# Performance work log

Measured on AMD Instinct MI355X. Metric: run time of the kernel, lower is better.

Reference implementation:

```python
import jax, jax.numpy as jnp
import numpy as np

BITS = 4
N_PACK = 8  # 32-bit container / 4-bit values
GROUPSIZE = 128
MASK = (1 << BITS) - 1


def _unpack(packed, n_valid):
    # packed: [R, ceil(n_valid/N_PACK)] int32 -> [R, n_valid] int32 nibbles
    shifts = (jnp.arange(N_PACK, dtype=jnp.int32) * BITS)
    vals = (packed[:, :, None] >> shifts) & MASK  # [R, C, N_PACK]
    return vals.reshape(packed.shape[0], -1)[:, :n_valid]


def setup_inputs() -> dict:
    key = jax.random.key(0)
    k0, k1, k2, k3, k4 = jax.random.split(key, 5)
    O, I = 4096, 4096
    ng = I // GROUPSIZE  # 32
    x = jax.random.normal(k0, (2, 2048, I), dtype=jnp.float32)
    packed_weight = jax.random.randint(k1, (O, I // N_PACK), 0, 2147483647, dtype=jnp.int32)
    scale = jax.random.uniform(k2, (O, ng), dtype=jnp.float32)
    packed_zp = jax.random.randint(k3, (O, (ng + N_PACK - 1) // N_PACK), 0, 2147483647, dtype=jnp.int32)
    bias = jax.random.normal(k4, (O,), dtype=jnp.float32)
    return {"x": x, "packed_weight": packed_weight, "scale": scale,
            "packed_zp": packed_zp, "bias": bias}


def reference(x, packed_weight, scale, packed_zp, bias):
    O, ng = scale.shape
    I = packed_weight.shape[1] * N_PACK
    # unpack uint4 weights and zero-points (matches torch recover(): shift+mask)
    w_int = _unpack(packed_weight, I)          # [O, I] values in [0, 15]
    zp_int = _unpack(packed_zp, ng)            # [O, ng]
    # per-group dequant: (w - zp) * scale
    w = w_int.reshape(O, ng, GROUPSIZE).astype(scale.dtype)
    fp_weight = ((w - zp_int[:, :, None].astype(scale.dtype)) * scale[:, :, None]).reshape(O, I)
    # F.linear: x @ W^T + b
    return jnp.einsum('bsi,oi->bso', x, fp_weight) + bias
```

## Files before the change

### kernel.cpp

```cpp
#include <hip/hip_runtime.h>
#include <stdint.h>

typedef __attribute__((ext_vector_type(4))) float  floatx4;
typedef __attribute__((ext_vector_type(8))) short  shortx8;
typedef __attribute__((ext_vector_type(4))) unsigned short ushortx4;

typedef unsigned int   u32;
typedef unsigned short u16;

#define TILE    128
#define BK      64
#define THREADS 256
#define CHUNK   (TILE * BK)

__device__ __forceinline__ u32 pack2bf(float f0, float f1) {
    u32 u0 = __builtin_bit_cast(u32, f0) + 0x8000u;
    u32 u1 = __builtin_bit_cast(u32, f1) + 0x8000u;
    return __builtin_amdgcn_perm(u1, u0, 0x07060302u);
}

__device__ __forceinline__ unsigned short f2bf(float f) {
    u32 u = __builtin_bit_cast(u32, f);
    u += 0x7FFFu + ((u >> 16) & 1u);
    return (unsigned short)(u >> 16);
}

__global__ __launch_bounds__(THREADS)
void prep_kernel(const float* __restrict__ x, const int* __restrict__ pw,
                 const float* __restrict__ scale, const int* __restrict__ pzp,
                 u16* __restrict__ At, u16* __restrict__ Bt,
                 int M, int O, int I, int ng, int lsSeg, int lsG) {
    const int NT = gridDim.x * THREADS;
    const int t0 = blockIdx.x * THREADS + threadIdx.x;
    const int segsPerRow = I >> 3;

    const int Sx = (M * I) >> 3;
    for (int s = t0; s < Sx; s += NT) {
        const float4 v0 = ((const float4*)x)[(size_t)s * 2];
        const float4 v1 = ((const float4*)x)[(size_t)s * 2 + 1];
        u32 p[4];
        p[0] = pack2bf(v0.x, v0.y); p[1] = pack2bf(v0.z, v0.w);
        p[2] = pack2bf(v1.x, v1.y); p[3] = pack2bf(v1.z, v1.w);
        ((uint4*)At)[s] = *(uint4*)p;
    }

    const int Sw = (O * I) >> 3;
    for (int s = t0; s < Sw; s += NT) {
        const u32 wq = (u32)pw[s];
        const int o    = s >> lsSeg;
        const int wcol = s & (segsPerRow - 1);
        const int g    = wcol >> lsG;
        const float sc = scale[o * ng + g];
        const int zpw  = pzp[o * ((ng + 7) >> 3) + (g >> 3)];
        const int zp   = (zpw >> ((g & 7) * 4)) & 15;
        const float nzc = -sc * (float)(zp + 128);
        float v[8];
        #pragma unroll
        for (int j = 0; j < 8; j++) {
            u32 tt;
            if (j < 4)       tt = (wq << (16 - 4 * j)) & 0x000F0000u;
            else if (j == 4) tt = wq & 0x000F0000u;
            else             tt = (wq >> (4 * j - 16)) & 0x000F0000u;
            v[j] = __builtin_fmaf(__builtin_bit_cast(float, tt | 0x43000000u), sc, nzc);
        }
        u32 p[4];
        p[0] = pack2bf(v[0], v[1]); p[1] = pack2bf(v[2], v[3]);
        p[2] = pack2bf(v[4], v[5]); p[3] = pack2bf(v[6], v[7]);
        ((uint4*)Bt)[s] = *(uint4*)p;
    }
}

__global__ __launch_bounds__(THREADS, 2)
void gemm_bf16(const u16* __restrict__ At, const u16* __restrict__ Bt,
               const float* __restrict__ bias, float* __restrict__ out,
               int O, int I, int KT) {
    __shared__ u16 As[CHUNK];
    __shared__ u16 Bs[CHUNK];

    const int tid = threadIdx.x;
    const int nblk_n = O / TILE;
    const int mt = blockIdx.x / nblk_n;
    const int nt = blockIdx.x % nblk_n;
    const int w = tid >> 6, lane = tid & 63;
    const int wm = w >> 1, wn = w & 1;
    const int l15 = lane & 15, l4 = lane >> 4;
    const int sw  = l15 & 7;

    const int sr = tid >> 3;
    const int sc = (tid & 7) ^ (sr & 7);

    floatx4 acc[4][4];
    #pragma unroll
    for (int i = 0; i < 4; i++)
        #pragma unroll
        for (int j = 0; j < 4; j++)
            acc[i][j] = (floatx4){0.f, 0.f, 0.f, 0.f};

    const u16* gaBase = At + ((size_t)(mt * TILE) + sr) * I + sc * 8;
    const u16* gbBase = Bt + ((size_t)(nt * TILE) + sr) * I + sc * 8;

    for (int kt = 0; kt < KT; kt++) {
        const u16* ga = gaBase + kt * BK;
        const u16* gb = gbBase + kt * BK;
        __syncthreads();
        #pragma unroll
        for (int it = 0; it < 4; it++) {
            const int ldsOff = it * 2048 + tid * 8;
            const size_t gOff = (size_t)(it * 32) * I;
            __builtin_amdgcn_global_load_lds((const __attribute__((address_space(1))) u32*)(ga + gOff),
                                             (__attribute__((address_space(3))) u32*)(As + ldsOff),
                                             16, 0, 0);
            __builtin_amdgcn_global_load_lds((const __attribute__((address_space(1))) u32*)(gb + gOff),
                                             (__attribute__((address_space(3))) u32*)(Bs + ldsOff),
                                             16, 0, 0);
        }
        __syncthreads();

        #pragma unroll
        for (int ks = 0; ks < 2; ks++) {
            shortx8 af[4], bf[4];
            #pragma unroll
            for (int i = 0; i < 4; i++)
                af[i] = *(const shortx8*)(&As[(wm * 64 + i * 16 + l15) * BK + ((ks * 4 + l4) ^ sw) * 8]);
            #pragma unroll
            for (int j = 0; j < 4; j++)
                bf[j] = *(const shortx8*)(&Bs[(wn * 64 + j * 16 + l15) * BK + ((ks * 4 + l4) ^ sw) * 8]);
            #pragma unroll
            for (int i = 0; i < 4; i++)
                #pragma unroll
                for (int j = 0; j < 4; j++)
                    acc[i][j] = __builtin_amdgcn_mfma_f32_16x16x32_bf16(af[i], bf[j], acc[i][j], 0, 0, 0);
        }
    }

    #pragma unroll
    for (int j = 0; j < 4; j++) {
        int col  = nt * TILE + wn * 64 + j * 16 + l15;
        float bv = bias[col];
        #pragma unroll
        for (int i = 0; i < 4; i++) {
            int rowb = mt * TILE + wm * 64 + i * 16 + l4 * 4;
            #pragma unroll
            for (int r = 0; r < 4; r++)
                out[(size_t)(rowb + r) * O + col] = acc[i][j][r] + bv;
        }
    }
}

#define LDA 72
__global__ __launch_bounds__(THREADS, 2)
void wql_fused(const float* __restrict__ x, const int* __restrict__ pw,
               const float* __restrict__ scale, const int* __restrict__ pzp,
               const float* __restrict__ bias, float* __restrict__ out,
               int M, int O, int I, int ng)
{
    __shared__ unsigned short As[TILE * LDA];
    __shared__ unsigned short Bs[TILE * LDA];
    const int tid = threadIdx.x;
    const int nblk_n = O / TILE;
    const int mt = blockIdx.x / nblk_n, nt = blockIdx.x % nblk_n;
    const int w = tid >> 6, lane = tid & 63;
    const int wm = w >> 1, wn = w & 1;
    const int l15 = lane & 15, l4 = lane >> 4;
    const int pw_rowlen = I / 8, zp_rowlen = (ng + 7) / 8, GS = I / ng;

    floatx4 acc[4][4];
    #pragma unroll
    for (int i = 0; i < 4; i++)
        #pragma unroll
        for (int j = 0; j < 4; j++) acc[i][j] = (floatx4){0.f, 0.f, 0.f, 0.f};

    const int nk = I / BK;
    for (int kt = 0; kt < nk; kt++) {
        __syncthreads();
        #pragma unroll
        for (int it = 0; it < 8; it++) {
            int f = tid + it * THREADS;
            int row = f >> 4, seg = f & 15;
            const float4 v = *(const float4*)(x + (size_t)(mt * TILE + row) * I + kt * BK + seg * 4);
            ushortx4 b;
            b.x = f2bf(v.x); b.y = f2bf(v.y); b.z = f2bf(v.z); b.w = f2bf(v.w);
            *(ushortx4*)(&As[row * LDA + seg * 4]) = b;
        }
        const int g = (kt * BK) / GS;
        #pragma unroll
        for (int it = 0; it < 4; it++) {
            int e = tid + it * THREADS;
            int row = e >> 3, c = e & 7;
            int o = nt * TILE + row;
            int wq = pw[(size_t)o * pw_rowlen + kt * (BK / 8) + c];
            float s = scale[o * ng + g];
            int zpw = pzp[o * zp_rowlen + (g >> 3)];
            int zp = (zpw >> ((g & 7) * 4)) & 15;
            shortx8 b;
            #pragma unroll
            for (int j = 0; j < 8; j++) {
                int nib = (wq >> (4 * j)) & 15;
                b[j] = (short)f2bf((float)(nib - zp) * s);
            }
            *(shortx8*)(&Bs[row * LDA + c * 8]) = b;
        }
        __syncthreads();
        #pragma unroll
        for (int ks = 0; ks < 2; ks++) {
            shortx8 af[4], bf[4];
            #pragma unroll
            for (int i = 0; i < 4; i++)
                af[i] = *(const shortx8*)(&As[(wm * 64 + i * 16 + l15) * LDA + ks * 32 + l4 * 8]);
            #pragma unroll
            for (int j = 0; j < 4; j++)
                bf[j] = *(const shortx8*)(&Bs[(wn * 64 + j * 16 + l15) * LDA + ks * 32 + l4 * 8]);
            #pragma unroll
            for (int i = 0; i < 4; i++)
                #pragma unroll
                for (int j = 0; j < 4; j++)
                    acc[i][j] = __builtin_amdgcn_mfma_f32_16x16x32_bf16(af[i], bf[j], acc[i][j], 0, 0, 0);
        }
    }
    #pragma unroll
    for (int j = 0; j < 4; j++) {
        int col = nt * TILE + wn * 64 + j * 16 + l15;
        float bv = bias[col];
        #pragma unroll
        for (int i = 0; i < 4; i++) {
            int rowb = mt * TILE + wm * 64 + i * 16 + l4 * 4;
            #pragma unroll
            for (int r = 0; r < 4; r++)
                out[(size_t)(rowb + r) * O + col] = acc[i][j][r] + bv;
        }
    }
}

extern "C" void kernel_launch(void* const* d_in, const int* in_sizes, int n_in,
                              void* d_out, int out_size, void* d_ws, size_t ws_size,
                              hipStream_t stream) {
    const float* x     = (const float*)d_in[0];
    const int*   pw    = (const int*)d_in[1];
    const float* scale = (const float*)d_in[2];
    const int*   pzp   = (const int*)d_in[3];
    const float* bias  = (const float*)d_in[4];
    float*       out   = (float*)d_out;

    const int O  = in_sizes[4];
    const int ng = in_sizes[2] / O;
    const int I  = (in_sizes[1] / O) * 8;
    const int M  = in_sizes[0] / I;
    const int KT = I / BK;
    int lsSeg = 0; { int v = I >> 3; while ((1 << lsSeg) < v) lsSeg++; }
    int lsG = 0;   { int v = (I / ng) >> 3; while ((1 << lsG) < v) lsG++; }

    const size_t need = ((size_t)M * I + (size_t)O * I) * sizeof(u16);
    if (ws_size >= need) {
        u16* At = (u16*)d_ws;
        u16* Bt = At + (size_t)M * I;
        prep_kernel<<<dim3(2048), THREADS, 0, stream>>>(x, pw, scale, pzp, At, Bt, M, O, I, ng, lsSeg, lsG);
        gemm_bf16<<<dim3((M / TILE) * (O / TILE)), THREADS, 0, stream>>>(At, Bt, bias, out, O, I, KT);
    } else {
        wql_fused<<<dim3((M / TILE) * (O / TILE)), THREADS, 0, stream>>>(x, pw, scale, pzp, bias, out, M, O, I, ng);
    }
}
```

Baseline: 252.8 us.

## Double-buffer LDS tiles in bf16 GEMM to overlap global loads with MFMA

The GEMM kernel gets two LDS buffers for A and B. It issues the direct-to-LDS loads for the next K tile before computing the current one, with a manual vmcnt wait and raw barriers. The aim is to hide global memory latency behind the MFMA work. LDS use doubles to 64KB per block, which may limit the two-blocks-per-CU occupancy, and the hand-written vmcnt count relies on exactly 8 outstanding loads per stage.

```diff
diff --git a/kernel.cpp b/kernel.cpp
--- a/kernel.cpp
+++ b/kernel.cpp
@@ -74,8 +74,8 @@
 void gemm_bf16(const u16* __restrict__ At, const u16* __restrict__ Bt,
                const float* __restrict__ bias, float* __restrict__ out,
                int O, int I, int KT) {
-    __shared__ u16 As[CHUNK];
-    __shared__ u16 Bs[CHUNK];
+    __shared__ u16 As[2][CHUNK];
+    __shared__ u16 Bs[2][CHUNK];
 
     const int tid = threadIdx.x;
     const int nblk_n = O / TILE;
@@ -98,40 +98,57 @@
 
     const u16* gaBase = At + ((size_t)(mt * TILE) + sr) * I + sc * 8;
     const u16* gbBase = Bt + ((size_t)(nt * TILE) + sr) * I + sc * 8;
-
-    for (int kt = 0; kt < KT; kt++) {
+    const int ldsOffBase = tid * 8;
+
+    auto issue = [&](int buf, int kt) {
         const u16* ga = gaBase + kt * BK;
         const u16* gb = gbBase + kt * BK;
-        __syncthreads();
         #pragma unroll
         for (int it = 0; it < 4; it++) {
-            const int ldsOff = it * 2048 + tid * 8;
+            const int ldsOff = it * 2048 + ldsOffBase;
             const size_t gOff = (size_t)(it * 32) * I;
             __builtin_amdgcn_global_load_lds((const __attribute__((address_space(1))) u32*)(ga + gOff),
-                                             (__attribute__((address_space(3))) u32*)(As + ldsOff),
+                                             (__attribute__((address_space(3))) u32*)(&As[buf][ldsOff]),
                                              16, 0, 0);
             __builtin_amdgcn_global_load_lds((const __attribute__((address_space(1))) u32*)(gb + gOff),
-                                             (__attribute__((address_space(3))) u32*)(Bs + ldsOff),
+                                             (__attribute__((address_space(3))) u32*)(&Bs[buf][ldsOff]),
                                              16, 0, 0);
         }
-        __syncthreads();
-
+    };
+
+    auto compute = [&](int buf) {
+        const u16* asb = As[buf];
+        const u16* bsb = Bs[buf];
         #pragma unroll
         for (int ks = 0; ks < 2; ks++) {
-            shortx8 af[4], bf[4];
-            #pragma unroll
-            for (int i = 0; i < 4; i++)
-                af[i] = *(const shortx8*)(&As[(wm * 64 + i * 16 + l15) * BK + ((ks * 4 + l4) ^ sw) * 8]);
+            shortx8 af[4], bfr[4];
+            #pragma unroll
+            for (int i = 0; i < 4; i++)
+                af[i] = *(const shortx8*)(&asb[(wm * 64 + i * 16 + l15) * BK + ((ks * 4 + l4) ^ sw) * 8]);
             #pragma unroll
             for (int j = 0; j < 4; j++)
-                bf[j] = *(const shortx8*)(&Bs[(wn * 64 + j * 16 + l15) * BK + ((ks * 4 + l4) ^ sw) * 8]);
+                bfr[j] = *(const shortx8*)(&bsb[(wn * 64 + j * 16 + l15) * BK + ((ks * 4 + l4) ^ sw) * 8]);
             #pragma unroll
             for (int i = 0; i < 4; i++)
                 #pragma unroll
                 for (int j = 0; j < 4; j++)
-                    acc[i][j] = __builtin_amdgcn_mfma_f32_16x16x32_bf16(af[i], bf[j], acc[i][j], 0, 0, 0);
-        }
-    }
+                    acc[i][j] = __builtin_amdgcn_mfma_f32_16x16x32_bf16(af[i], bfr[j], acc[i][j], 0, 0, 0);
+        }
+    };
+
+    issue(0, 0);
+    int cur = 0;
+    for (int kt = 0; kt < KT - 1; kt++) {
+        issue(cur ^ 1, kt + 1);
+        asm volatile("s_waitcnt vmcnt(8)" ::: "memory");
+        __builtin_amdgcn_s_barrier();
+        compute(cur);
+        __builtin_amdgcn_s_barrier();
+        cur ^= 1;
+    }
+    asm volatile("s_waitcnt vmcnt(0)" ::: "memory");
+    __builtin_amdgcn_s_barrier();
+    compute(cur);
 
     #pragma unroll
     for (int j = 0; j < 4; j++) {
@@ -203,18 +220,18 @@
         __syncthreads();
         #pragma unroll
         for (int ks = 0; ks < 2; ks++) {
-            shortx8 af[4], bf[4];
+            shortx8 af[4], bfr[4];
             #pragma unroll
             for (int i = 0; i < 4; i++)
                 af[i] = *(const shortx8*)(&As[(wm * 64 + i * 16 + l15) * LDA + ks * 32 + l4 * 8]);
             #pragma unroll
             for (int j = 0; j < 4; j++)
-                bf[j] = *(const shortx8*)(&Bs[(wn * 64 + j * 16 + l15) * LDA + ks * 32 + l4 * 8]);
+                bfr[j] = *(const shortx8*)(&Bs[(wn * 64 + j * 16 + l15) * LDA + ks * 32 + l4 * 8]);
             #pragma unroll
             for (int i = 0; i < 4; i++)
                 #pragma unroll
                 for (int j = 0; j < 4; j++)
-                    acc[i][j] = __builtin_amdgcn_mfma_f32_16x16x32_bf16(af[i], bf[j], acc[i][j], 0, 0, 0);
+                    acc[i][j] = __builtin_amdgcn_mfma_f32_16x16x32_bf16(af[i], bfr[j], acc[i][j], 0, 0, 0);
         }
     }
     #pragma unroll
```

New measurement: 269.2 us. +6.5%, slower.

## Add 256x256-tile 512-thread GEMM with 4-stage LDS pipeline and XCD block remap

Applied to the files above, without the earlier changes.

Adds a new bf16 GEMM kernel using 256x256 output tiles, 8 waves and a 4-deep LDS ring buffer. Async global-to-LDS loads for future k-steps are issued between MFMA phases, with explicit vmcnt waits, split barriers and s_setprio raised around the MFMA blocks. Block IDs are remapped so that groups of eight consecutive workgroups land on the same XCD's tile neighbourhood to improve L2 reuse. The larger tile lowers global traffic per FLOP and the deep pipeline is meant to hide load latency. The cost is 128KB of LDS and heavier register pressure, which limit occupancy.

```diff
diff --git a/kernel.cpp b/kernel.cpp
--- a/kernel.cpp
+++ b/kernel.cpp
@@ -70,6 +70,132 @@
     }
 }
 
+#define VM8 asm volatile("s_waitcnt vmcnt(8)" ::: "memory")
+#define VM4 asm volatile("s_waitcnt vmcnt(4)" ::: "memory")
+#define VM0 asm volatile("s_waitcnt vmcnt(0)" ::: "memory")
+
+#define GTILE(T, DOISS, WAITSTMT) do {                                                    \
+    const u16* __restrict__ sb = &S[((T) & 3) * 16384];                                   \
+    u16* nb = &S[(((T) + 3) & 3) * 16384];                                                \
+    shortx8 af[4], bfr[4];                                                                \
+    _Pragma("unroll")                                                                     \
+    for (int i = 0; i < 4; i++) af[i]  = *(const shortx8*)(sb + rdA + i * 1024);          \
+    _Pragma("unroll")                                                                     \
+    for (int j = 0; j < 4; j++) bfr[j] = *(const shortx8*)(sb + rdB + j * 1024);          \
+    if (DOISS) {                                                                          \
+        _Pragma("unroll")                                                                 \
+        for (int l = 0; l < 2; l++)                                                       \
+            __builtin_amdgcn_global_load_lds((const __attribute__((address_space(1))) u32*)(g[l]), \
+                (__attribute__((address_space(3))) u32*)(nb + ldsoff[l]), 16, 0, 0);      \
+    }                                                                                     \
+    __builtin_amdgcn_s_barrier();                                                         \
+    __builtin_amdgcn_s_setprio(1);                                                        \
+    _Pragma("unroll")                                                                     \
+    for (int i = 0; i < 4; i++)                                                           \
+        _Pragma("unroll")                                                                 \
+        for (int j = 0; j < 4; j++)                                                       \
+            acc[i][j] = __builtin_amdgcn_mfma_f32_16x16x32_bf16(af[i], bfr[j], acc[i][j], 0, 0, 0); \
+    __builtin_amdgcn_s_setprio(0);                                                        \
+    __builtin_amdgcn_s_barrier();                                                         \
+    _Pragma("unroll")                                                                     \
+    for (int i = 0; i < 4; i++) af[i] = *(const shortx8*)(sb + rdA + 4096 + i * 1024);    \
+    if (DOISS) {                                                                          \
+        _Pragma("unroll")                                                                 \
+        for (int l = 2; l < 4; l++)                                                       \
+            __builtin_amdgcn_global_load_lds((const __attribute__((address_space(1))) u32*)(g[l]), \
+                (__attribute__((address_space(3))) u32*)(nb + ldsoff[l]), 16, 0, 0);      \
+        _Pragma("unroll")                                                                 \
+        for (int l = 0; l < 4; l++) g[l] += 32;                                           \
+    }                                                                                     \
+    __builtin_amdgcn_s_barrier();                                                         \
+    __builtin_amdgcn_s_setprio(1);                                                        \
+    _Pragma("unroll")                                                                     \
+    for (int i = 0; i < 4; i++)                                                           \
+        _Pragma("unroll")                                                                 \
+        for (int j = 0; j < 4; j++)                                                       \
+            acc[i + 4][j] = __builtin_amdgcn_mfma_f32_16x16x32_bf16(af[i], bfr[j], acc[i + 4][j], 0, 0, 0); \
+    __builtin_amdgcn_s_setprio(0);                                                        \
+    WAITSTMT;                                                                             \
+    __builtin_amdgcn_s_barrier();                                                         \
+} while (0)
+
+__global__ __launch_bounds__(512, 2)
+void gemm256(const u16* __restrict__ At, const u16* __restrict__ Bt,
+             const float* __restrict__ bias, float* __restrict__ out,
+             int O, int I, int KT) {
+    __shared__ u16 S[4 * 16384];
+
+    const int tid = threadIdx.x;
+    const int nblk_n = O / 256;
+
+    int bid = blockIdx.x;
+    const int nwg = gridDim.x;
+    if ((nwg & 7) == 0) {
+        const int q = nwg >> 3;
+        bid = (bid & 7) * q + (bid >> 3);
+    }
+    const int mt = bid / nblk_n, nt = bid % nblk_n;
+
+    const int w = tid >> 6, lane = tid & 63;
+    const int wm = w >> 2, wn = w & 3;
+    const int l15 = lane & 15, l4 = lane >> 4;
+    const int sw  = l15 & 7;
+
+    const int rdA = (wm * 128 + l15) * 64 + ((l4 ^ sw) * 8);
+    const int rdB = (wn * 64  + l15) * 64 + ((((l4 | 4) ^ sw)) * 8);
+
+    const u16* g[4];
+    int ldsoff[4];
+    #pragma unroll
+    for (int l = 0; l < 4; l++) {
+        const int s   = (w * 4 + l) * 64 + lane;
+        const int row = s >> 3;
+        const int k   = (s & 7) ^ (row & 7);
+        ldsoff[l] = (w * 4 + l) * 512 + lane * 8;
+        g[l] = (k < 4) ? (At + (size_t)(mt * 256 + row) * I + k * 8)
+                       : (Bt + (size_t)(nt * 256 + row) * I + (k - 4) * 8);
+    }
+
+    floatx4 acc[8][4];
+    #pragma unroll
+    for (int i = 0; i < 8; i++)
+        #pragma unroll
+        for (int j = 0; j < 4; j++)
+            acc[i][j] = (floatx4){0.f, 0.f, 0.f, 0.f};
+
+    #pragma unroll
+    for (int p = 0; p < 3; p++) {
+        u16* sb = &S[p * 16384];
+        #pragma unroll
+        for (int l = 0; l < 4; l++)
+            __builtin_amdgcn_global_load_lds((const __attribute__((address_space(1))) u32*)(g[l]),
+                (__attribute__((address_space(3))) u32*)(sb + ldsoff[l]), 16, 0, 0);
+        #pragma unroll
+        for (int l = 0; l < 4; l++) g[l] += 32;
+    }
+    VM8;
+    __builtin_amdgcn_s_barrier();
+
+    int t = 0;
+    for (; t < KT - 3; ++t) GTILE(t, 1, VM8);
+    GTILE(t, 0, VM4); ++t;
+    GTILE(t, 0, VM0); ++t;
+    GTILE(t, 0, (void)0);
+
+    #pragma unroll
+    for (int j = 0; j < 4; j++) {
+        int col  = nt * 256 + wn * 64 + j * 16 + l15;
+        float bv = bias[col];
+        #pragma unroll
+        for (int i = 0; i < 8; i++) {
+            int rowb = mt * 256 + wm * 128 + i * 16 + l4 * 4;
+            #pragma unroll
+            for (int r = 0; r < 4; r++)
+                out[(size_t)(rowb + r) * O + col] = acc[i][j][r] + bv;
+        }
+    }
+}
+
 __global__ __launch_bounds__(THREADS, 2)
 void gemm_bf16(const u16* __restrict__ At, const u16* __restrict__ Bt,
                const float* __restrict__ bias, float* __restrict__ out,
@@ -118,18 +244,18 @@
 
         #pragma unroll
         for (int ks = 0; ks < 2; ks++) {
-            shortx8 af[4], bf[4];
+            shortx8 af[4], bfr[4];
             #pragma unroll
             for (int i = 0; i < 4; i++)
                 af[i] = *(const shortx8*)(&As[(wm * 64 + i * 16 + l15) * BK + ((ks * 4 + l4) ^ sw) * 8]);
             #pragma unroll
             for (int j = 0; j < 4; j++)
-                bf[j] = *(const shortx8*)(&Bs[(wn * 64 + j * 16 + l15) * BK + ((ks * 4 + l4) ^ sw) * 8]);
+                bfr[j] = *(const shortx8*)(&Bs[(wn * 64 + j * 16 + l15) * BK + ((ks * 4 + l4) ^ sw) * 8]);
             #pragma unroll
             for (int i = 0; i < 4; i++)
                 #pragma unroll
                 for (int j = 0; j < 4; j++)
-                    acc[i][j] = __builtin_amdgcn_mfma_f32_16x16x32_bf16(af[i], bf[j], acc[i][j], 0, 0, 0);
+                    acc[i][j] = __builtin_amdgcn_mfma_f32_16x16x32_bf16(af[i], bfr[j], acc[i][j], 0, 0, 0);
         }
     }
 
@@ -203,18 +329,18 @@
         __syncthreads();
         #pragma unroll
         for (int ks = 0; ks < 2; ks++) {
-            shortx8 af[4], bf[4];
+            shortx8 af[4], bfr[4];
             #pragma unroll
             for (int i = 0; i < 4; i++)
                 af[i] = *(const shortx8*)(&As[(wm * 64 + i * 16 + l15) * LDA + ks * 32 + l4 * 8]);
             #pragma unroll
             for (int j = 0; j < 4; j++)
-                bf[j] = *(const shortx8*)(&Bs[(wn * 64 + j * 16 + l15) * LDA + ks * 32 + l4 * 8]);
+                bfr[j] = *(const shortx8*)(&Bs[(wn * 64 + j * 16 + l15) * LDA + ks * 32 + l4 * 8]);
             #pragma unroll
             for (int i = 0; i < 4; i++)
                 #pragma unroll
                 for (int j = 0; j < 4; j++)
-                    acc[i][j] = __builtin_amdgcn_mfma_f32_16x16x32_bf16(af[i], bf[j], acc[i][j], 0, 0, 0);
+                    acc[i][j] = __builtin_amdgcn_mfma_f32_16x16x32_bf16(af[i], bfr[j], acc[i][j], 0, 0, 0);
         }
     }
     #pragma unroll
@@ -245,7 +371,6 @@
     const int ng = in_sizes[2] / O;
     const int I  = (in_sizes[1] / O) * 8;
     const int M  = in_sizes[0] / I;
-    const int KT = I / BK;
     int lsSeg = 0; { int v = I >> 3; while ((1 << lsSeg) < v) lsSeg++; }
     int lsG = 0;   { int v = (I / ng) >> 3; while ((1 << lsG) < v) lsG++; }
 
@@ -254,7 +379,12 @@
         u16* At = (u16*)d_ws;
         u16* Bt = At + (size_t)M * I;
         prep_kernel<<<dim3(2048), THREADS, 0, stream>>>(x, pw, scale, pzp, At, Bt, M, O, I, ng, lsSeg, lsG);
-        gemm_bf16<<<dim3((M / TILE) * (O / TILE)), THREADS, 0, stream>>>(At, Bt, bias, out, O, I, KT);
+        const bool ok256 = (M % 256 == 0) && (O % 256 == 0) && (I % 32 == 0) && (I / 32 >= 8);
+        if (ok256) {
+            gemm256<<<dim3((M / 256) * (O / 256)), 512, 0, stream>>>(At, Bt, bias, out, O, I, I / 32);
+        } else {
+            gemm_bf16<<<dim3((M / TILE) * (O / TILE)), THREADS, 0, stream>>>(At, Bt, bias, out, O, I, I / BK);
+        }
     } else {
         wql_fused<<<dim3((M / TILE) * (O / TILE)), THREADS, 0, stream>>>(x, pw, scale, pzp, bias, out, M, O, I, ng);
     }
```

Result: no change. 257.1 us (+1.7%).

## Add 256x256 double-buffered bf16 GEMM with interleaved LDS staging and MFMA

Applied to the files above, without the earlier changes.

Adds a new 512-thread GEMM kernel that computes 256x256 output tiles. It uses a 128KB double-buffered LDS layout and interleaves async global-to-LDS loads with MFMA quadrants, using explicit waitcnt, sched_barrier and setprio. A grouped block-index remap is meant to improve L2 reuse. The larger tile is meant to raise arithmetic intensity and hide load latency behind compute, at the cost of heavy register and LDS use, which limits occupancy.

```diff
diff --git a/kernel.cpp b/kernel.cpp
--- a/kernel.cpp
+++ b/kernel.cpp
@@ -70,6 +70,139 @@
     }
 }
 
+
+#define BARR  __builtin_amdgcn_s_barrier()
+#define SCB0  __builtin_amdgcn_sched_barrier(0)
+#define PRI1  __builtin_amdgcn_s_setprio(1)
+#define PRI0  __builtin_amdgcn_s_setprio(0)
+#define LGKM(N) asm volatile("s_waitcnt lgkmcnt(" #N ")" ::: "memory")
+#define VMC(N)  asm volatile("s_waitcnt vmcnt(" #N ")" ::: "memory")
+
+#define GLL(GP, LP)                                                                        \
+    __builtin_amdgcn_global_load_lds((const __attribute__((address_space(1))) u32*)(GP),   \
+        (__attribute__((address_space(3))) u32*)(LP), 16, 0, 0)
+
+#define STGA(HOFFE, LB) do { GLL(pA0 + (HOFFE), S + (LB) + tid * 8);                       \
+                             GLL(pA1 + (HOFFE), S + (LB) + 4096 + tid * 8); } while (0)
+#define STGB(HOFFE, LB) do { GLL(pB0 + (HOFFE), S + (LB) + tid * 8);                       \
+                             GLL(pB1 + (HOFFE), S + (LB) + 4096 + tid * 8); } while (0)
+
+#define RDA(DST, BUF, H) do { _Pragma("unroll")                                            \
+    for (int i = 0; i < 4; i++) {                                                          \
+        DST[i][0] = *(const shortx8*)(S + (BUF)*32768 + (H)*16384 + aoff + i*1024 + c0);   \
+        DST[i][1] = *(const shortx8*)(S + (BUF)*32768 + (H)*16384 + aoff + i*1024 + c1);   \
+    } } while (0)
+#define RDB(DST, BUF, H) do { _Pragma("unroll")                                            \
+    for (int j = 0; j < 2; j++) {                                                          \
+        DST[j][0] = *(const shortx8*)(S + (BUF)*32768 + (H)*16384 + 8192 + boff + j*1024 + c0); \
+        DST[j][1] = *(const shortx8*)(S + (BUF)*32768 + (H)*16384 + 8192 + boff + j*1024 + c1); \
+    } } while (0)
+
+#define MFQ(AR, BR, RO, CO) do { _Pragma("unroll")                                         \
+    for (int i = 0; i < 4; i++) { _Pragma("unroll")                                        \
+        for (int j = 0; j < 2; j++) {                                                      \
+            acc[(RO)+i][(CO)+j] = __builtin_amdgcn_mfma_f32_16x16x32_bf16(                 \
+                AR[i][0], BR[j][0], acc[(RO)+i][(CO)+j], 0, 0, 0);                         \
+            acc[(RO)+i][(CO)+j] = __builtin_amdgcn_mfma_f32_16x16x32_bf16(                 \
+                AR[i][1], BR[j][1], acc[(RO)+i][(CO)+j], 0, 0, 0);                         \
+        } } } while (0)
+
+#define WINDOW(BUF, DOSTG, LAST, W1S, W4S) do {                                            \
+                       \
+    RDA(a1, BUF, 1);                                                                       \
+    if (DOSTG) { STGA(0, ((BUF)^1)*32768);                                                 \
+                 STGB(0, ((BUF)^1)*32768 + 8192); }                                        \
+    BARR; LGKM(8); SCB0; PRI1; MFQ(a0, b0, 0, 0); PRI0; W1S; BARR;                         \
+                                     \
+    RDB(b1, BUF, 1);                                                                       \
+    if (DOSTG) STGA(hOff, ((BUF)^1)*32768 + 16384);                                        \
+    BARR; LGKM(4); SCB0; PRI1; MFQ(a1, b0, 4, 0); PRI0; VMC(4); BARR;                      \
+                                                   \
+    if (DOSTG) STGB(hOff, ((BUF)^1)*32768 + 16384 + 8192);                                 \
+    BARR; LGKM(0); SCB0; PRI1; MFQ(a0, b1, 0, 2); PRI0; VMC(4); BARR;                      \
+                                        \
+    if (!(LAST)) { RDA(a0, (BUF)^1, 0); RDB(b0, (BUF)^1, 0); LGKM(8); }                    \
+    BARR; SCB0; PRI1; MFQ(a1, b1, 4, 2); PRI0; W4S; BARR;                                  \
+    if (DOSTG) { pA0 += 64; pA1 += 64; pB0 += 64; pB1 += 64; }                             \
+} while (0)
+
+__global__ __launch_bounds__(512, 2)
+void gemm256(const u16* __restrict__ At, const u16* __restrict__ Bt,
+             const float* __restrict__ bias, float* __restrict__ out,
+             int O, int I, int KT) {
+    __shared__ u16 S[65536];
+
+    const int tid = threadIdx.x;
+    const int nblk_n = O / 256;
+
+    int bid = blockIdx.x;
+    const int nwg = gridDim.x;
+    if ((nwg & 7) == 0) {
+        const int q = nwg >> 3;
+        bid = (bid & 7) * q + (bid >> 3);
+    }
+    const int mt = bid / nblk_n, nt = bid % nblk_n;
+
+    const int w = tid >> 6, lane = tid & 63;
+    const int wm = w >> 2, wn = w & 3;
+    const int l15 = lane & 15, l4 = lane >> 4;
+    const int sw  = l15 & 7;
+
+    const int aoff = (wm * 64 + l15) * 64;
+    const int boff = (wn * 32 + l15) * 64;
+    const int c0 = ((0 * 4 + l4) ^ sw) * 8;
+    const int c1 = ((1 * 4 + l4) ^ sw) * 8;
+
+    const int rs = tid >> 3;
+    const int ks = (tid & 7) ^ (rs & 7);
+    const u16* pA0 = At + ((size_t)(mt * 256) + rs) * I + ks * 8;
+    const u16* pA1 = pA0 + (size_t)64 * I;
+    const u16* pB0 = Bt + ((size_t)(nt * 256) + rs) * I + ks * 8;
+    const u16* pB1 = pB0 + (size_t)64 * I;
+    const size_t hOff = (size_t)128 * I;
+
+    floatx4 acc[8][4];
+    #pragma unroll
+    for (int i = 0; i < 8; i++)
+        #pragma unroll
+        for (int j = 0; j < 4; j++)
+            acc[i][j] = (floatx4){0.f, 0.f, 0.f, 0.f};
+
+    shortx8 a0[4][2], a1[4][2], b0[2][2], b1[2][2];
+
+    STGA(0, 0);
+    STGB(0, 8192);
+    STGA(hOff, 16384);
+    STGB(hOff, 16384 + 8192);
+    pA0 += 64; pA1 += 64; pB0 += 64; pB1 += 64;
+    VMC(0);
+    BARR;
+    RDA(a0, 0, 0);
+    RDB(b0, 0, 0);
+
+    const int pairs = (KT - 2) >> 1;
+    #pragma unroll 1
+    for (int t2 = 0; t2 < pairs; ++t2) {
+        WINDOW(0, 1, 0, VMC(4), VMC(2));
+        WINDOW(1, 1, 0, VMC(4), VMC(2));
+    }
+    WINDOW(0, 1, 0, VMC(4), VMC(2));
+    WINDOW(1, 0, 1, VMC(0), (void)0);
+
+    #pragma unroll
+    for (int j = 0; j < 4; j++) {
+        int col  = nt * 256 + (j >> 1) * 128 + wn * 32 + (j & 1) * 16 + l15;
+        float bv = bias[col];
+        #pragma unroll
+        for (int i = 0; i < 8; i++) {
+            int rowb = mt * 256 + (i >> 2) * 128 + wm * 64 + (i & 3) * 16 + l4 * 4;
+            #pragma unroll
+            for (int r = 0; r < 4; r++)
+                out[(size_t)(rowb + r) * O + col] = acc[i][j][r] + bv;
+        }
+    }
+}
+
 __global__ __launch_bounds__(THREADS, 2)
 void gemm_bf16(const u16* __restrict__ At, const u16* __restrict__ Bt,
                const float* __restrict__ bias, float* __restrict__ out,
@@ -107,29 +240,25 @@
         for (int it = 0; it < 4; it++) {
             const int ldsOff = it * 2048 + tid * 8;
             const size_t gOff = (size_t)(it * 32) * I;
-            __builtin_amdgcn_global_load_lds((const __attribute__((address_space(1))) u32*)(ga + gOff),
-                                             (__attribute__((address_space(3))) u32*)(As + ldsOff),
-                                             16, 0, 0);
-            __builtin_amdgcn_global_load_lds((const __attribute__((address_space(1))) u32*)(gb + gOff),
-                                             (__attribute__((address_space(3))) u32*)(Bs + ldsOff),
-                                             16, 0, 0);
+            GLL(ga + gOff, As + ldsOff);
+            GLL(gb + gOff, Bs + ldsOff);
         }
         __syncthreads();
 
         #pragma unroll
-        for (int ks = 0; ks < 2; ks++) {
-            shortx8 af[4], bf[4];
+        for (int kss = 0; kss < 2; kss++) {
+            shortx8 af[4], bfr2[4];
             #pragma unroll
             for (int i = 0; i < 4; i++)
-                af[i] = *(const shortx8*)(&As[(wm * 64 + i * 16 + l15) * BK + ((ks * 4 + l4) ^ sw) * 8]);
+                af[i] = *(const shortx8*)(&As[(wm * 64 + i * 16 + l15) * BK + ((kss * 4 + l4) ^ sw) * 8]);
             #pragma unroll
             for (int j = 0; j < 4; j++)
-                bf[j] = *(const shortx8*)(&Bs[(wn * 64 + j * 16 + l15) * BK + ((ks * 4 + l4) ^ sw) * 8]);
+                bfr2[j] = *(const shortx8*)(&Bs[(wn * 64 + j * 16 + l15) * BK + ((kss * 4 + l4) ^ sw) * 8]);
             #pragma unroll
             for (int i = 0; i < 4; i++)
                 #pragma unroll
                 for (int j = 0; j < 4; j++)
-                    acc[i][j] = __builtin_amdgcn_mfma_f32_16x16x32_bf16(af[i], bf[j], acc[i][j], 0, 0, 0);
+                    acc[i][j] = __builtin_amdgcn_mfma_f32_16x16x32_bf16(af[i], bfr2[j], acc[i][j], 0, 0, 0);
         }
     }
 
@@ -202,19 +331,19 @@
         }
         __syncthreads();
         #pragma unroll
-        for (int ks = 0; ks < 2; ks++) {
-            shortx8 af[4], bf[4];
+        for (int kss = 0; kss < 2; kss++) {
+            shortx8 af[4], bfr2[4];
             #pragma unroll
             for (int i = 0; i < 4; i++)
-                af[i] = *(const shortx8*)(&As[(wm * 64 + i * 16 + l15) * LDA + ks * 32 + l4 * 8]);
+                af[i] = *(const shortx8*)(&As[(wm * 64 + i * 16 + l15) * LDA + kss * 32 + l4 * 8]);
             #pragma unroll
             for (int j = 0; j < 4; j++)
-                bf[j] = *(const shortx8*)(&Bs[(wn * 64 + j * 16 + l15) * LDA + ks * 32 + l4 * 8]);
+                bfr2[j] = *(const shortx8*)(&Bs[(wn * 64 + j * 16 + l15) * LDA + kss * 32 + l4 * 8]);
             #pragma unroll
             for (int i = 0; i < 4; i++)
                 #pragma unroll
                 for (int j = 0; j < 4; j++)
-                    acc[i][j] = __builtin_amdgcn_mfma_f32_16x16x32_bf16(af[i], bf[j], acc[i][j], 0, 0, 0);
+                    acc[i][j] = __builtin_amdgcn_mfma_f32_16x16x32_bf16(af[i], bfr2[j], acc[i][j], 0, 0, 0);
         }
     }
     #pragma unroll
@@ -245,7 +374,6 @@
     const int ng = in_sizes[2] / O;
     const int I  = (in_sizes[1] / O) * 8;
     const int M  = in_sizes[0] / I;
-    const int KT = I / BK;
     int lsSeg = 0; { int v = I >> 3; while ((1 << lsSeg) < v) lsSeg++; }
     int lsG = 0;   { int v = (I / ng) >> 3; while ((1 << lsG) < v) lsG++; }
 
@@ -254,7 +382,13 @@
         u16* At = (u16*)d_ws;
         u16* Bt = At + (size_t)M * I;
         prep_kernel<<<dim3(2048), THREADS, 0, stream>>>(x, pw, scale, pzp, At, Bt, M, O, I, ng, lsSeg, lsG);
-        gemm_bf16<<<dim3((M / TILE) * (O / TILE)), THREADS, 0, stream>>>(At, Bt, bias, out, O, I, KT);
+        const int KT64 = I / 64;
+        const bool ok256 = (M % 256 == 0) && (O % 256 == 0) && (I % 128 == 0) && (KT64 >= 4);
+        if (ok256) {
+            gemm256<<<dim3((M / 256) * (O / 256)), 512, 0, stream>>>(At, Bt, bias, out, O, I, KT64);
+        } else {
+            gemm_bf16<<<dim3((M / TILE) * (O / TILE)), THREADS, 0, stream>>>(At, Bt, bias, out, O, I, I / BK);
+        }
     } else {
         wql_fused<<<dim3((M / TILE) * (O / TILE)), THREADS, 0, stream>>>(x, pw, scale, pzp, bias, out, M, O, I, ng);
     }
```

Result: slower. 425.9 us (+68.4%).
